# Optimization experiments

Measured on AMD Instinct MI355X. Metric: run time of the kernel, lower is better.

Reference implementation:

```python
import jax, jax.numpy as jnp
import numpy as np

H = 256; NL = 6; N = 64; DCONV = 4; DIN = 512; HEADS = 8; P = 64
CONVD = DIN + 2 * N            # 640
PROJ = 2 * DIN + 2 * N + HEADS  # 1160


def rmsnorm(x, w, eps=1e-6):
    return x * jax.lax.rsqrt(jnp.mean(x * x, axis=-1, keepdims=True) + eps) * w


def mamba2(x, Win, conv_w, conv_b, dt_bias, A_log, D, gnorm, Wout):
    # x: (b, l, H)
    b, l, _ = x.shape
    zxbcdt = x @ Win                       # (b, l, PROJ)
    z = zxbcdt[..., :DIN]
    xBC = zxbcdt[..., DIN:DIN + CONVD]
    dt = zxbcdt[..., DIN + CONVD:]         # (b, l, HEADS)
    # causal depthwise conv1d along l
    xp = jnp.pad(xBC, ((0, 0), (DCONV - 1, 0), (0, 0)))
    xc = conv_b + sum(xp[:, k:k + l, :] * conv_w[k] for k in range(DCONV))
    xBC = jax.nn.silu(xc)
    xs = xBC[..., :DIN]
    B = xBC[..., DIN:DIN + N]
    C = xBC[..., DIN + N:]
    dt = jax.nn.softplus(dt + dt_bias)
    dA = jnp.exp(dt * (-jnp.exp(A_log)))   # (b, l, HEADS)
    xh = xs.reshape(b, l, HEADS, P)
    xdt = xh * dt[..., None]

    def step(h, inp):
        dA_t, xdt_t, B_t, C_t = inp
        h = dA_t[:, :, None, None] * h + xdt_t[..., None] * B_t[:, None, None, :]
        return h, jnp.einsum('bhpn,bn->bhp', h, C_t)

    h0 = jnp.zeros((b, HEADS, P, N), x.dtype)
    _, ys = jax.lax.scan(step, h0, (jnp.swapaxes(dA, 0, 1), jnp.swapaxes(xdt, 0, 1),
                                    jnp.swapaxes(B, 0, 1), jnp.swapaxes(C, 0, 1)))
    y = jnp.swapaxes(ys, 0, 1) + D[None, None, :, None] * xh   # (b, l, HEADS, P)
    y = y.reshape(b, l, DIN) * jax.nn.silu(z)
    return rmsnorm(y, gnorm) @ Wout


def dual_path(x, t_norm, t_Win, t_cw, t_cb, t_dtb, t_Alog, t_D, t_gn, t_Wout,
              b_norm, b_Win, b_cw, b_cb, b_dtb, b_Alog, b_D, b_gn, b_Wout):
    batch, time, bands, hdim = x.shape
    for i in range(NL):
        # time-axis pass (raw row-major reshape, matching torch .reshape semantics)
        xt = x.reshape(batch * bands, time, hdim)
        xt = xt + mamba2(rmsnorm(xt, t_norm[i]), t_Win[i], t_cw[i], t_cb[i],
                         t_dtb[i], t_Alog[i], t_D[i], t_gn[i], t_Wout[i])
        x = jnp.swapaxes(xt.reshape(batch, bands, time, hdim), 1, 2)
        # band-axis pass
        xb = x.reshape(batch * time, bands, hdim)
        xb = xb + mamba2(rmsnorm(xb, b_norm[i]), b_Win[i], b_cw[i], b_cb[i],
                         b_dtb[i], b_Alog[i], b_D[i], b_gn[i], b_Wout[i])
        x = xb.reshape(batch, time, bands, hdim)
    return x


def setup_inputs() -> dict:
    key = jax.random.key(0)
    ks = jax.random.split(key, 3)
    x = jax.random.normal(ks[0], (2, 512, 64, H), jnp.float32)

    def make_params(k):
        kk = jax.random.split(k, 5)
        g = lambda kx, sh, s: jax.random.normal(kx, sh, jnp.float32) * s
        return dict(
            norm=jnp.ones((NL, H), jnp.float32),
            Win=g(kk[0], (NL, H, PROJ), H ** -0.5),
            cw=g(kk[1], (NL, DCONV, CONVD), 0.2),
            cb=jnp.zeros((NL, CONVD), jnp.float32),
            dtb=g(kk[2], (NL, HEADS), 0.5),
            Alog=jnp.log(jnp.abs(g(kk[3], (NL, HEADS), 1.0)) + 0.5),
            D=jnp.ones((NL, HEADS), jnp.float32),
            gn=jnp.ones((NL, DIN), jnp.float32),
            Wout=g(kk[4], (NL, DIN, H), DIN ** -0.5),
        )

    tp = make_params(ks[1]); bp = make_params(ks[2])
    out = {'x': x}
    for name, d in (('t', tp), ('b', bp)):
        for kname, v in d.items():
            out[f'{name}_{kname}'] = v
    return out


def reference(x, t_norm, t_Win, t_cw, t_cb, t_dtb, t_Alog, t_D, t_gn, t_Wout,
              b_norm, b_Win, b_cw, b_cb, b_dtb, b_Alog, b_D, b_gn, b_Wout):
    return dual_path(x, t_norm, t_Win, t_cw, t_cb, t_dtb, t_Alog, t_D, t_gn, t_Wout,
                     b_norm, b_Win, b_cw, b_cb, b_dtb, b_Alog, b_D, b_gn, b_Wout)
```

## Files before the change

kernel.cpp:

```cpp
#include <hip/hip_runtime.h>
#include <math.h>

#define NLAY   6
#define Hd     256
#define DINv   512
#define NHEADS 8
#define CONVDv 640
#define PROJv  1160
#define ZW     656
#define NTOK   65536
#define NCH    1024

typedef __attribute__((ext_vector_type(8))) short bf16x8;
typedef __attribute__((ext_vector_type(4))) float f32x4;
typedef unsigned short u16;

__device__ __forceinline__ float siluf(float v) {
    return v * __builtin_amdgcn_rcpf(1.0f + __expf(-v));
}
__device__ __forceinline__ float bflo(unsigned u) { return __uint_as_float(u << 16); }
__device__ __forceinline__ float bfhi(unsigned u) { return __uint_as_float(u & 0xffff0000u); }
__device__ __forceinline__ u16 f2b(float f) {
    unsigned u = __float_as_uint(f);
    return (u16)((u + 0x7fffu + ((u >> 16) & 1u)) >> 16);
}
__device__ __forceinline__ float b2f(u16 s) { return __uint_as_float(((unsigned)s) << 16); }

__device__ __forceinline__ void gl_lds16(const void* g, void* l) {
    __builtin_amdgcn_global_load_lds((const __attribute__((address_space(1))) unsigned int*)g,
                                     (__attribute__((address_space(3))) unsigned int*)l, 16, 0, 0);
}

__global__ __launch_bounds__(512)
void kprep_win(const float* __restrict__ tW, const float* __restrict__ bW,
               u16* __restrict__ Whi, u16* __restrict__ Wlo)
{
    const int li = blockIdx.y, j = blockIdx.x;
    const int t  = threadIdx.x;
    const int kk = t >> 6, col = (t >> 2) & 15, quad = t & 3;
    const float* W = (li < 6) ? (tW + (size_t)li * Hd * PROJv)
                              : (bW + (size_t)(li - 6) * Hd * PROJv);
    const int fullcol = 16 * j + col;
    const size_t ob = ((size_t)li * 74 + j) * 4096 + kk * 512 + quad * 128 + col * 8;
#pragma unroll
    for (int e = 0; e < 8; e++) {
        const int k = kk * 32 + quad * 8 + e;
        const float v = (fullcol < PROJv) ? W[(size_t)k * PROJv + fullcol] : 0.f;
        const u16 hi = f2b(v);
        Whi[ob + e] = hi;
        Wlo[ob + e] = f2b(v - b2f(hi));
    }
}

__global__ __launch_bounds__(512)
void kprep_wout(const float* __restrict__ tW, const float* __restrict__ tg,
                const float* __restrict__ bW, const float* __restrict__ bg,
                u16* __restrict__ Whi, u16* __restrict__ Wlo)
{
    const int li = blockIdx.y, j = blockIdx.x;
    const int t  = threadIdx.x;
    const int kk = t >> 5, col = (t >> 1) & 15, qh = t & 1;
    const float* W = (li < 6) ? tW + (size_t)li * DINv * Hd : bW + (size_t)(li - 6) * DINv * Hd;
    const float* g = (li < 6) ? tg + li * DINv : bg + (li - 6) * DINv;
    const int fullcol = 16 * j + col;
#pragma unroll
    for (int q = 0; q < 2; q++) {
        const int quad = qh * 2 + q;
        const size_t ob = ((size_t)li * 16 + j) * 8192 + kk * 512 + quad * 128 + col * 8;
#pragma unroll
        for (int e = 0; e < 8; e++) {
            const int k = kk * 32 + quad * 8 + e;
            const float v = W[(size_t)k * Hd + fullcol] * g[k];
            const u16 hi = f2b(v);
            Whi[ob + e] = hi;
            Wlo[ob + e] = f2b(v - b2f(hi));
        }
    }
}

__global__ __launch_bounds__(512, 4)
void k1_mfma(const float* __restrict__ src, u16* __restrict__ zs,
             u16* __restrict__ xrawT, u16* __restrict__ bnd,
             const float* __restrict__ nw,
             const u16* __restrict__ Whi, const u16* __restrict__ Wlo)
{
    __shared__ __align__(16) char smem[67584];
    u16* sAh = (u16*)smem;
    u16* sAl = sAh + 64 * 264;
    const int tid = threadIdx.x;
    const int cb  = blockIdx.x;
    const int R0  = cb * 64;

    {
        const int tok = tid >> 3, l8 = tid & 7;
        const float* xr = src + ((size_t)(R0 + tok)) * Hd + l8 * 32;
        float vv[32];
#pragma unroll
        for (int q = 0; q < 8; q++) {
            float4 v = ((const float4*)xr)[q];
            vv[4*q] = v.x; vv[4*q+1] = v.y; vv[4*q+2] = v.z; vv[4*q+3] = v.w;
        }
        float ss = 0.f;
#pragma unroll
        for (int j = 0; j < 32; j++) ss += vv[j] * vv[j];
#pragma unroll
        for (int m = 4; m >= 1; m >>= 1) ss += __shfl_xor(ss, m, 8);
        const float rstd = rsqrtf(ss * (1.0f / Hd) + 1e-6f);
        const float* nr = nw + l8 * 32;
        u16* dh = sAh + tok * 264 + l8 * 32;
        u16* dl = sAl + tok * 264 + l8 * 32;
#pragma unroll
        for (int j = 0; j < 32; j++) {
            const float val = vv[j] * rstd * nr[j];
            const u16 hi = f2b(val);
            dh[j] = hi;
            dl[j] = f2b(val - b2f(hi));
        }
    }
    __syncthreads();

    const int lane = tid & 63, wave = tid >> 6;
    const int rh = wave >> 1, cw = wave & 1;
    const int quad = lane >> 4, m16 = lane & 15;

    bf16x8 ah[8], al[8];
    {
        const u16* ph = sAh + (rh * 16 + m16) * 264 + quad * 8;
        const u16* pl = sAl + (rh * 16 + m16) * 264 + quad * 8;
#pragma unroll
        for (int kk = 0; kk < 8; kk++) {
            ah[kk] = *(const bf16x8*)(ph + kk * 32);
            al[kk] = *(const bf16x8*)(pl + kk * 32);
        }
    }
    __syncthreads();

    u16* sW = (u16*)smem;

#define K1_STAGE(p, buf)                                                          \
    {                                                                             \
        const int obase = wave * 4096;                                            \
        _Pragma("unroll")                                                         \
        for (int i = 0; i < 4; i++) {                                             \
            const int o = obase + i * 1024;                                       \
            const int chunk = o >> 13, t2 = chunk >> 1, hl = chunk & 1;           \
            const int within = o & 8191;                                          \
            const u16* sbase = (hl ? Wlo : Whi) + (size_t)(2 * (p) + t2) * 4096;  \
            gl_lds16((const char*)sbase + within + lane * 16,                     \
                     (char*)sW + (buf) * 32768 + o);                              \
        }                                                                         \
    }

    K1_STAGE(0, 0);
    __syncthreads();

    for (int p = 0; p < 37; p++) {
        if (p < 36) K1_STAGE(p + 1, (p + 1) & 1);
        const int j = 2 * p + cw;
        const u16* tb = sW + (p & 1) * 16384 + cw * 8192 + lane * 8;
        f32x4 acc = (f32x4){0.f, 0.f, 0.f, 0.f};
#pragma unroll
        for (int kk = 0; kk < 8; kk++) {
            bf16x8 bh = *(const bf16x8*)(tb + kk * 512);
            bf16x8 bl = *(const bf16x8*)(tb + 4096 + kk * 512);
            acc = __builtin_amdgcn_mfma_f32_16x16x32_bf16(ah[kk], bh, acc, 0, 0, 0);
            acc = __builtin_amdgcn_mfma_f32_16x16x32_bf16(al[kk], bh, acc, 0, 0, 0);
            acc = __builtin_amdgcn_mfma_f32_16x16x32_bf16(ah[kk], bl, acc, 0, 0, 0);
        }
        const int fullcol = 16 * j + m16;
        if (j < 32) {
            u16* zr = zs + (size_t)(R0 + rh * 16 + quad * 4) * ZW + fullcol;
#pragma unroll
            for (int i = 0; i < 4; i++) zr[(size_t)i * ZW] = f2b(acc[i]);
        } else if (j < 64) {
            const int ch = fullcol - 512;
            uint2 v;
            v.x = (unsigned)f2b(acc[0]) | ((unsigned)f2b(acc[1]) << 16);
            v.y = (unsigned)f2b(acc[2]) | ((unsigned)f2b(acc[3]) << 16);
            *(uint2*)(xrawT + ((size_t)cb * 512 + ch) * 64 + rh * 16 + quad * 4) = v;
            if (rh == 3 && quad == 3) {
#pragma unroll
                for (int i = 1; i < 4; i++)
                    bnd[((size_t)cb * 3 + (i - 1)) * 640 + ch] = f2b(acc[i]);
            }
        } else if (j < 73) {
            const int zc = fullcol - 512;
            u16* zr = zs + (size_t)(R0 + rh * 16 + quad * 4) * ZW + zc;
#pragma unroll
            for (int i = 0; i < 4; i++) zr[(size_t)i * ZW] = f2b(acc[i]);
            if (j < 72 && rh == 3 && quad == 3) {
#pragma unroll
                for (int i = 1; i < 4; i++)
                    bnd[((size_t)cb * 3 + (i - 1)) * 640 + zc] = f2b(acc[i]);
            }
        }
        __syncthreads();
    }
#undef K1_STAGE
}

__device__ __forceinline__ void conv32_rmw(u16* xp, float w0, float w1, float w2, float w3,
                                           float bias, float h3, float h2, float h1)
{
    uint4 va = ((const uint4*)xp)[0], vb = ((const uint4*)xp)[1],
          vc = ((const uint4*)xp)[2], vd = ((const uint4*)xp)[3];
    unsigned uu[16] = {va.x, va.y, va.z, va.w, vb.x, vb.y, vb.z, vb.w,
                       vc.x, vc.y, vc.z, vc.w, vd.x, vd.y, vd.z, vd.w};
    unsigned ou[16];
#pragma unroll
    for (int k = 0; k < 16; k++) {
        const float x0 = bflo(uu[k]);
        const u16 o0 = f2b(siluf(bias + w0*h3 + w1*h2 + w2*h1 + w3*x0));
        h3 = h2; h2 = h1; h1 = x0;
        const float x1 = bfhi(uu[k]);
        const u16 o1 = f2b(siluf(bias + w0*h3 + w1*h2 + w2*h1 + w3*x1));
        h3 = h2; h2 = h1; h1 = x1;
        ou[k] = (unsigned)o0 | ((unsigned)o1 << 16);
    }
    ((uint4*)xp)[0] = make_uint4(ou[0],  ou[1],  ou[2],  ou[3]);
    ((uint4*)xp)[1] = make_uint4(ou[4],  ou[5],  ou[6],  ou[7]);
    ((uint4*)xp)[2] = make_uint4(ou[8],  ou[9],  ou[10], ou[11]);
    ((uint4*)xp)[3] = make_uint4(ou[12], ou[13], ou[14], ou[15]);
}

__global__ __launch_bounds__(256, 4)
void k2a_conv(u16* __restrict__ zs, u16* __restrict__ xrawT,
              float* __restrict__ spb, const u16* __restrict__ bnd,
              const float* __restrict__ cwp, const float* __restrict__ cbp,
              const float* __restrict__ dtbp, const float* __restrict__ alogp, int L)
{
    __shared__ __align__(16) u16 sBC[64][128];
    const int tid = threadIdx.x;
    const int cb  = blockIdx.x;
    const size_t row0 = (size_t)cb * 64;
    const bool atStart = (((int)(row0 % (size_t)L)) == 0);
    const int lane = tid & 63, wave = tid >> 6;

#pragma unroll
    for (int j = 0; j < 4; j++) {
        const int t0 = wave * 16 + j * 4;
        gl_lds16(zs + (row0 + t0 + (lane >> 4)) * ZW + 512 + (lane & 15) * 8,
                 (char*)sBC + t0 * 256);
    }

#pragma unroll
    for (int cc = 0; cc < 2; cc++) {
        const int ch = tid + cc * 256;
        const float w0 = cwp[0*CONVDv + ch], w1 = cwp[1*CONVDv + ch],
                    w2 = cwp[2*CONVDv + ch], w3 = cwp[3*CONVDv + ch];
        u16* xp = xrawT + ((size_t)cb * 512 + ch) * 64 + 32;
        const uint2 hv = *(const uint2*)(xp - 4);
        conv32_rmw(xp, w0, w1, w2, w3, cbp[ch], bfhi(hv.x), bflo(hv.y), bfhi(hv.y));
    }

    if (tid < 64) {
        const int t = tid;
        const uint4 dv = *(const uint4*)(zs + (row0 + t) * ZW + 640);
        const unsigned uu[4] = {dv.x, dv.y, dv.z, dv.w};
        float sp[8], ld[8];
#pragma unroll
        for (int h = 0; h < 8; h++) {
            const float d = ((h & 1) ? bfhi(uu[h >> 1]) : bflo(uu[h >> 1])) + dtbp[h];
            const float s = (d > 20.f) ? d : __logf(1.f + __expf(d));
            sp[h] = s;
            ld[h] = -__expf(alogp[h]) * s;
        }
        float* ob = spb + (row0 + t) * 24;
        *(float4*)(ob)      = make_float4(sp[0], sp[1], sp[2], sp[3]);
        *(float4*)(ob + 4)  = make_float4(sp[4], sp[5], sp[6], sp[7]);
        *(float4*)(ob + 8)  = make_float4(ld[0], ld[1], ld[2], ld[3]);
        *(float4*)(ob + 12) = make_float4(ld[4], ld[5], ld[6], ld[7]);
    }
    __syncthreads();

#pragma unroll
    for (int cc = 0; cc < 2; cc++) {
        const int ch = tid + cc * 256;
        const float w0 = cwp[0*CONVDv + ch], w1 = cwp[1*CONVDv + ch],
                    w2 = cwp[2*CONVDv + ch], w3 = cwp[3*CONVDv + ch];
        float h1 = 0.f, h2 = 0.f, h3 = 0.f;
        if (!atStart) {
            const u16* bp = bnd + ((size_t)(cb - 1) * 3) * 640 + ch;
            h3 = b2f(bp[0]); h2 = b2f(bp[640]); h1 = b2f(bp[1280]);
        }
        conv32_rmw(xrawT + ((size_t)cb * 512 + ch) * 64, w0, w1, w2, w3, cbp[ch], h3, h2, h1);
    }

    u16 o[32];
    {
        const int ch  = tid & 127;
        const int th  = tid >> 7;
        const int t0  = th * 32;
        const int gch = 512 + ch;
        const float w0 = cwp[0*CONVDv + gch], w1 = cwp[1*CONVDv + gch],
                    w2 = cwp[2*CONVDv + gch], w3 = cwp[3*CONVDv + gch];
        const float bias = cbp[gch];
        float h1, h2, h3;
        if (th) {
            h3 = b2f(sBC[29][ch]); h2 = b2f(sBC[30][ch]); h1 = b2f(sBC[31][ch]);
        } else if (!atStart) {
            const u16* bp = bnd + ((size_t)(cb - 1) * 3) * 640 + gch;
            h3 = b2f(bp[0]); h2 = b2f(bp[640]); h1 = b2f(bp[1280]);
        } else { h1 = h2 = h3 = 0.f; }
#pragma unroll
        for (int t = 0; t < 32; t++) {
            const float xv = b2f(sBC[t0 + t][ch]);
            o[t] = f2b(siluf(bias + w0*h3 + w1*h2 + w2*h1 + w3*xv));
            h3 = h2; h2 = h1; h1 = xv;
        }
    }
    __syncthreads();
    {
        const int ch = tid & 127, t0 = (tid >> 7) * 32;
#pragma unroll
        for (int t = 0; t < 32; t++) sBC[t0 + t][ch] = o[t];
    }
    __syncthreads();
#pragma unroll
    for (int i = 0; i < 4; i++) {
        const int g = tid + i * 256;
        const int t = g >> 4, s16 = g & 15;
        *(uint4*)(zs + (row0 + t) * ZW + 512 + s16 * 8) = *(const uint4*)(&sBC[t][s16 * 8]);
    }
}

template<bool TMODE>
__global__ __launch_bounds__(256, 3)
void k2b_ssd(u16* __restrict__ zs, u16* __restrict__ xrawT,
             float* __restrict__ spb, u16* __restrict__ Sbuf,
             const float* __restrict__ Dp)
{
    __shared__ __align__(16) float sG[64][68];
    __shared__ float sClog[NHEADS][64];
    __shared__ float sSp[NHEADS][64];
    __shared__ float sWd[NHEADS][64];
    __shared__ __align__(16) u16 sBT[64][72];
    const int tid = threadIdx.x;
    const int lane = tid & 63, wave = tid >> 6;
    const int quad = lane >> 4, m16 = lane & 15;
    const int cb = blockIdx.x;
    const size_t row0 = (size_t)cb * 64;

    if (TMODE) {
        const int t_ = tid >> 2, ns = (tid & 3) * 16;
        const u16* br = zs + (row0 + t_) * ZW + 512 + ns;
        uint4 a = ((const uint4*)br)[0], b = ((const uint4*)br)[1];
        unsigned uu[8] = {a.x, a.y, a.z, a.w, b.x, b.y, b.z, b.w};
#pragma unroll
        for (int k = 0; k < 8; k++) {
            sBT[ns + 2*k][t_]     = (u16)(uu[k] & 0xffff);
            sBT[ns + 2*k + 1][t_] = (u16)(uu[k] >> 16);
        }
    }

    {
        const u16* cp = zs + (row0 + 16 * wave + m16) * ZW + 576 + quad * 8;
        bf16x8 cf0 = *(const bf16x8*)(cp);
        bf16x8 cf1 = *(const bf16x8*)(cp + 32);
#pragma unroll
        for (int st = 0; st < 4; st++) {
            const u16* bp = zs + (row0 + 16 * st + m16) * ZW + 512 + quad * 8;
            f32x4 acc = (f32x4){0.f, 0.f, 0.f, 0.f};
            acc = __builtin_amdgcn_mfma_f32_16x16x32_bf16(cf0, *(const bf16x8*)(bp), acc, 0, 0, 0);
            acc = __builtin_amdgcn_mfma_f32_16x16x32_bf16(cf1, *(const bf16x8*)(bp + 32), acc, 0, 0, 0);
#pragma unroll
            for (int i = 0; i < 4; i++)
                sG[16 * wave + quad * 4 + i][16 * st + m16] = acc[i];
        }
    }

#pragma unroll
    for (int hh = 0; hh < 2; hh++) {
        const int h = wave * 2 + hh;
        float c = spb[(row0 + lane) * 24 + 8 + h];
        const float sp = spb[(row0 + lane) * 24 + h];
#pragma unroll
        for (int d = 1; d < 64; d <<= 1) {
            const float o = __shfl_up(c, d, 64);
            if (lane >= d) c += o;
        }
        sClog[h][lane] = c;
        sSp[h][lane] = sp;
        if (TMODE) {
            spb[(row0 + lane) * 24 + 16 + h] = __expf(c);
            const float cl63 = __shfl(c, 63, 64);
            sWd[h][lane] = __expf(cl63 - c) * sp;
        }
    }
    __syncthreads();

    if (TMODE) {
        for (int h = 0; h < NHEADS; h++) {
            bf16x8 Ahi[2], Alo[2];
#pragma unroll
            for (int kk = 0; kk < 2; kk++) {
                const u16* xp = xrawT + ((size_t)cb * 512 + h * 64 + 16 * wave + m16) * 64
                                + 32 * kk + quad * 8;
                bf16x8 xf = *(const bf16x8*)xp;
                const float* wp = &sWd[h][32 * kk + quad * 8];
#pragma unroll
                for (int j = 0; j < 8; j++) {
                    const float v = b2f((u16)xf[j]) * wp[j];
                    const u16 hi = f2b(v);
                    Ahi[kk][j] = (short)hi;
                    Alo[kk][j] = (short)f2b(v - b2f(hi));
                }
            }
            u16* sb = Sbuf + ((size_t)cb * 8 + h) * 4096;
#pragma unroll
            for (int nt = 0; nt < 4; nt++) {
                f32x4 acc = (f32x4){0.f, 0.f, 0.f, 0.f};
#pragma unroll
                for (int kk = 0; kk < 2; kk++) {
                    const bf16x8 bf_ = *(const bf16x8*)(&sBT[16 * nt + m16][32 * kk + quad * 8]);
                    acc = __builtin_amdgcn_mfma_f32_16x16x32_bf16(Ahi[kk], bf_, acc, 0, 0, 0);
                    acc = __builtin_amdgcn_mfma_f32_16x16x32_bf16(Alo[kk], bf_, acc, 0, 0, 0);
                }
#pragma unroll
                for (int i = 0; i < 4; i++)
                    sb[(16 * wave + quad * 4 + i) * 64 + 16 * nt + m16] = f2b(acc[i]);
            }
        }
        __syncthreads();
    }

    const int t = 16 * wave + m16;
    for (int h = 0; h < NHEADS; h++) {
        const float Dh = Dp[h];
        const float clt = sClog[h][t];
        bf16x8 Mhi[2], Mlo[2];
#pragma unroll
        for (int kk = 0; kk < 2; kk++) {
            const float* gp = &sG[t][32 * kk + quad * 8];
            const float* cp = &sClog[h][32 * kk + quad * 8];
            const float* pp = &sSp[h][32 * kk + quad * 8];
#pragma unroll
            for (int j = 0; j < 8; j++) {
                const int s = 32 * kk + quad * 8 + j;
                float m = (s <= t) ? (__expf(clt - cp[j]) * pp[j] * gp[j]) : 0.f;
                if (s == t) m += Dh;
                const u16 hi = f2b(m);
                Mhi[kk][j] = (short)hi;
                Mlo[kk][j] = (short)f2b(m - b2f(hi));
            }
        }
        bf16x8 xf[4][2];
#pragma unroll
        for (int pt = 0; pt < 4; pt++)
#pragma unroll
            for (int kk = 0; kk < 2; kk++)
                xf[pt][kk] = *(const bf16x8*)(xrawT
                    + ((size_t)cb * 512 + h * 64 + 16 * pt + m16) * 64 + 32 * kk + quad * 8);
        if (TMODE) __syncthreads();
        f32x4 accY[4];
#pragma unroll
        for (int pt = 0; pt < 4; pt++) {
            accY[pt] = (f32x4){0.f, 0.f, 0.f, 0.f};
#pragma unroll
            for (int kk = 0; kk < 2; kk++) {
                accY[pt] = __builtin_amdgcn_mfma_f32_16x16x32_bf16(Mhi[kk], xf[pt][kk], accY[pt], 0, 0, 0);
                accY[pt] = __builtin_amdgcn_mfma_f32_16x16x32_bf16(Mlo[kk], xf[pt][kk], accY[pt], 0, 0, 0);
            }
        }
#pragma unroll
        for (int pt = 0; pt < 4; pt++) {
            if (TMODE) {
                uint2 v;
                v.x = (unsigned)f2b(accY[pt][0]) | ((unsigned)f2b(accY[pt][1]) << 16);
                v.y = (unsigned)f2b(accY[pt][2]) | ((unsigned)f2b(accY[pt][3]) << 16);
                *(uint2*)(xrawT + ((size_t)cb * 512 + h * 64 + 16 * pt + m16) * 64
                          + 16 * wave + quad * 4) = v;
            } else {
#pragma unroll
                for (int i = 0; i < 4; i++) {
                    const size_t row = row0 + 16 * wave + quad * 4 + i;
                    const int col = h * 64 + 16 * pt + m16;
                    const u16 zv = zs[row * ZW + col];
                    zs[row * ZW + col] = f2b(accY[pt][i] * siluf(b2f(zv)));
                }
            }
        }
    }
}

__global__ __launch_bounds__(64, 4)
void k2c_states(u16* __restrict__ Sbuf, const float* __restrict__ spb)
{
    const int p = threadIdx.x, h = blockIdx.y, s = blockIdx.x;
    float H[64];
#pragma unroll
    for (int n = 0; n < 64; n++) H[n] = 0.f;
    for (int c = 1; c < 8; c++) {
        const float P = spb[((size_t)s * 512 + (c - 1) * 64 + 63) * 24 + 16 + h];
        u16* sp_ = Sbuf + (((size_t)(s * 8 + c - 1) * 8 + h) * 4096) + p * 64;
#pragma unroll
        for (int n = 0; n < 64; n += 8) {
            uint4 v = *(const uint4*)(sp_ + n);
            unsigned uu[4] = {v.x, v.y, v.z, v.w};
            float sv[8];
#pragma unroll
            for (int w2 = 0; w2 < 4; w2++) { sv[2*w2] = bflo(uu[w2]); sv[2*w2+1] = bfhi(uu[w2]); }
#pragma unroll
            for (int e = 0; e < 8; e++) H[n + e] = fmaf(P, H[n + e], sv[e]);
            uint4 o;
            o.x = (unsigned)f2b(H[n+0]) | ((unsigned)f2b(H[n+1]) << 16);
            o.y = (unsigned)f2b(H[n+2]) | ((unsigned)f2b(H[n+3]) << 16);
            o.z = (unsigned)f2b(H[n+4]) | ((unsigned)f2b(H[n+5]) << 16);
            o.w = (unsigned)f2b(H[n+6]) | ((unsigned)f2b(H[n+7]) << 16);
            *(uint4*)(sp_ + n) = o;
        }
    }
}

__global__ __launch_bounds__(256, 4)
void k2d_corr(u16* __restrict__ zs, const u16* __restrict__ xrawT,
              const float* __restrict__ spb, const u16* __restrict__ Sbuf)
{
    const int tid = threadIdx.x;
    const int lane = tid & 63, wave = tid >> 6;
    const int quad = lane >> 4, m16 = lane & 15;
    const int cb = blockIdx.x;
    const int c = cb & 7;
    const size_t row0 = (size_t)cb * 64;

    for (int h = 0; h < NHEADS; h++) {
        f32x4 acc[4];
#pragma unroll
        for (int pt = 0; pt < 4; pt++) {
            const uint2 v = *(const uint2*)(xrawT
                + ((size_t)cb * 512 + h * 64 + 16 * pt + m16) * 64 + 16 * wave + quad * 4);
            acc[pt][0] = bflo(v.x); acc[pt][1] = bfhi(v.x);
            acc[pt][2] = bflo(v.y); acc[pt][3] = bfhi(v.y);
        }
        if (c) {
            const float at = spb[(row0 + 16 * wave + m16) * 24 + 16 + h];
            bf16x8 Ahi[2], Alo[2];
#pragma unroll
            for (int kk = 0; kk < 2; kk++) {
                const u16* cp = zs + (row0 + 16 * wave + m16) * ZW + 576 + 32 * kk + quad * 8;
                bf16x8 cf = *(const bf16x8*)cp;
#pragma unroll
                for (int j = 0; j < 8; j++) {
                    const float v = b2f((u16)cf[j]) * at;
                    const u16 hi = f2b(v);
                    Ahi[kk][j] = (short)hi;
                    Alo[kk][j] = (short)f2b(v - b2f(hi));
                }
            }
            const u16* hb = Sbuf + ((size_t)(cb - 1) * 8 + h) * 4096;
#pragma unroll
            for (int pt = 0; pt < 4; pt++) {
#pragma unroll
                for (int kk = 0; kk < 2; kk++) {
                    bf16x8 hf = *(const bf16x8*)(hb + (16 * pt + m16) * 64 + 32 * kk + quad * 8);
                    acc[pt] = __builtin_amdgcn_mfma_f32_16x16x32_bf16(Ahi[kk], hf, acc[pt], 0, 0, 0);
                    acc[pt] = __builtin_amdgcn_mfma_f32_16x16x32_bf16(Alo[kk], hf, acc[pt], 0, 0, 0);
                }
            }
        }
#pragma unroll
        for (int pt = 0; pt < 4; pt++) {
#pragma unroll
            for (int i = 0; i < 4; i++) {
                const size_t row = row0 + 16 * wave + quad * 4 + i;
                const int col = h * 64 + 16 * pt + m16;
                const u16 zv = zs[row * ZW + col];
                zs[row * ZW + col] = f2b(acc[pt][i] * siluf(b2f(zv)));
            }
        }
    }
}

template<bool TMODE>
__global__ __launch_bounds__(256, 2)
void k3_mfma(const u16* __restrict__ zs, const float* __restrict__ src,
             float* __restrict__ dst,
             const u16* __restrict__ Whi, const u16* __restrict__ Wlo)
{
    __shared__ __align__(16) char smem[32768];
    const int tid = threadIdx.x;
    const int cb  = blockIdx.x;
    const int R0  = cb * 64;
    const int lane = tid & 63, wave = tid >> 6;
    const int quad = lane >> 4, m16 = lane & 15;

#define K3_STAGE(hc)                                                              \
    {                                                                             \
        const int jj = (hc) >> 1;                                                 \
        const char* wb = (const char*)((((hc) & 1) ? Wlo : Whi) + (size_t)jj * 8192); \
        char* db = smem + ((hc) & 1) * 16384 + wave * 4096;                       \
        _Pragma("unroll")                                                         \
        for (int i = 0; i < 4; i++)                                               \
            gl_lds16(wb + wave * 4096 + i * 1024 + lane * 16, db + i * 1024);     \
    }

    K3_STAGE(0);

    const u16* yr = zs + (size_t)(R0 + wave * 16 + m16) * ZW + quad * 8;
    float ss = 0.f;
#pragma unroll
    for (int kk = 0; kk < 16; kk++) {
        uint4 u = *(const uint4*)(yr + kk * 32);
        float a;
        a = bflo(u.x); ss += a * a;  a = bfhi(u.x); ss += a * a;
        a = bflo(u.y); ss += a * a;  a = bfhi(u.y); ss += a * a;
        a = bflo(u.z); ss += a * a;  a = bfhi(u.z); ss += a * a;
        a = bflo(u.w); ss += a * a;  a = bfhi(u.w); ss += a * a;
    }
    ss += __shfl_xor(ss, 16, 64);
    ss += __shfl_xor(ss, 32, 64);
    const float rstd = rsqrtf(ss * (1.0f / DINv) + 1e-6f);

    bf16x8 ah[16], al[16];
#pragma unroll
    for (int kk = 0; kk < 16; kk++) {
        uint4 u = *(const uint4*)(yr + kk * 32);
        unsigned w0 = u.x, w1 = u.y, w2 = u.z, w3 = u.w;
        float a, b;
        u16 hi;
        a = bflo(w0) * rstd; b = bfhi(w0) * rstd;
        hi = f2b(a); ah[kk][0] = (short)hi; al[kk][0] = (short)f2b(a - b2f(hi));
        hi = f2b(b); ah[kk][1] = (short)hi; al[kk][1] = (short)f2b(b - b2f(hi));
        a = bflo(w1) * rstd; b = bfhi(w1) * rstd;
        hi = f2b(a); ah[kk][2] = (short)hi; al[kk][2] = (short)f2b(a - b2f(hi));
        hi = f2b(b); ah[kk][3] = (short)hi; al[kk][3] = (short)f2b(b - b2f(hi));
        a = bflo(w2) * rstd; b = bfhi(w2) * rstd;
        hi = f2b(a); ah[kk][4] = (short)hi; al[kk][4] = (short)f2b(a - b2f(hi));
        hi = f2b(b); ah[kk][5] = (short)hi; al[kk][5] = (short)f2b(b - b2f(hi));
        a = bflo(w3) * rstd; b = bfhi(w3) * rstd;
        hi = f2b(a); ah[kk][6] = (short)hi; al[kk][6] = (short)f2b(a - b2f(hi));
        hi = f2b(b); ah[kk][7] = (short)hi; al[kk][7] = (short)f2b(b - b2f(hi));
    }
    __syncthreads();

    for (int j = 0; j < 16; j++) {
        K3_STAGE(2 * j + 1);
        f32x4 acc = (f32x4){0.f, 0.f, 0.f, 0.f};
        const u16* tb0 = (const u16*)smem + lane * 8;
#pragma unroll
        for (int kk = 0; kk < 16; kk++) {
            bf16x8 bh = *(const bf16x8*)(tb0 + kk * 512);
            acc = __builtin_amdgcn_mfma_f32_16x16x32_bf16(ah[kk], bh, acc, 0, 0, 0);
            acc = __builtin_amdgcn_mfma_f32_16x16x32_bf16(al[kk], bh, acc, 0, 0, 0);
        }
        __syncthreads();
        if (j < 15) K3_STAGE(2 * j + 2);
        const u16* tb1 = (const u16*)(smem + 16384) + lane * 8;
#pragma unroll
        for (int kk = 0; kk < 16; kk++) {
            bf16x8 bl = *(const bf16x8*)(tb1 + kk * 512);
            acc = __builtin_amdgcn_mfma_f32_16x16x32_bf16(ah[kk], bl, acc, 0, 0, 0);
        }
        {
            const int col = 16 * j + m16;
#pragma unroll
            for (int i = 0; i < 4; i++) {
                const size_t inrow = (size_t)(R0 + wave * 16 + quad * 4 + i);
                const float v = acc[i] + src[inrow * Hd + col];
                size_t orow;
                if (TMODE) {
                    const size_t sq = inrow >> 9;
                    const size_t tt = inrow & 511;
                    orow = ((sq >> 6) * 512 + tt) * 64 + (sq & 63);
                } else {
                    orow = inrow;
                }
                dst[orow * Hd + col] = v;
            }
        }
        __syncthreads();
    }
#undef K3_STAGE
}

extern "C" void kernel_launch(void* const* d_in, const int* in_sizes, int n_in,
                              void* d_out, int out_size, void* d_ws, size_t ws_size,
                              hipStream_t stream) {
    const float* x      = (const float*)d_in[0];
    const float* t_norm = (const float*)d_in[1];
    const float* t_Win  = (const float*)d_in[2];
    const float* t_cw   = (const float*)d_in[3];
    const float* t_cb   = (const float*)d_in[4];
    const float* t_dtb  = (const float*)d_in[5];
    const float* t_Alog = (const float*)d_in[6];
    const float* t_D    = (const float*)d_in[7];
    const float* t_gn   = (const float*)d_in[8];
    const float* t_Wout = (const float*)d_in[9];
    const float* b_norm = (const float*)d_in[10];
    const float* b_Win  = (const float*)d_in[11];
    const float* b_cw   = (const float*)d_in[12];
    const float* b_cb   = (const float*)d_in[13];
    const float* b_dtb  = (const float*)d_in[14];
    const float* b_Alog = (const float*)d_in[15];
    const float* b_D    = (const float*)d_in[16];
    const float* b_gn   = (const float*)d_in[17];
    const float* b_Wout = (const float*)d_in[18];

    float* out = (float*)d_out;
    char*  wsb = (char*)d_ws;
    float* xbuf = (float*)wsb;
    u16*   Sbuf = (u16*)wsb;
    size_t off = 67108864;
    u16* W1hi = (u16*)(wsb + off); off += (size_t)12 * 74 * 4096 * 2;
    u16* W1lo = (u16*)(wsb + off); off += (size_t)12 * 74 * 4096 * 2;
    u16* W2hi = (u16*)(wsb + off); off += (size_t)12 * 16 * 8192 * 2;
    u16* W2lo = (u16*)(wsb + off); off += (size_t)12 * 16 * 8192 * 2;
    u16* zs   = (u16*)(wsb + off); off += (size_t)NTOK * ZW * 2;
    float* spb = (float*)(wsb + off); off += (size_t)NTOK * 24 * 4;
    u16* xrawT = (u16*)(wsb + off); off += (size_t)NTOK * 512 * 2;
    u16* bnd  = (u16*)(wsb + off);

    kprep_win<<<dim3(74, 12), 512, 0, stream>>>(t_Win, b_Win, W1hi, W1lo);
    kprep_wout<<<dim3(16, 12), 512, 0, stream>>>(t_Wout, t_gn, b_Wout, b_gn, W2hi, W2lo);

    for (int i = 0; i < NLAY; i++) {
        const float* src_t = (i == 0) ? x : out;
        k1_mfma<<<NCH, 512, 0, stream>>>(src_t, zs, xrawT, bnd, t_norm + i * Hd,
                 W1hi + (size_t)i * 74 * 4096, W1lo + (size_t)i * 74 * 4096);
        k2a_conv<<<NCH, 256, 0, stream>>>(zs, xrawT, spb, bnd,
                 t_cw + i * 4 * CONVDv, t_cb + i * CONVDv, t_dtb + i * NHEADS,
                 t_Alog + i * NHEADS, 512);
        k2b_ssd<true><<<NCH, 256, 0, stream>>>(zs, xrawT, spb, Sbuf, t_D + i * NHEADS);
        k2c_states<<<dim3(128, NHEADS), 64, 0, stream>>>(Sbuf, spb);
        k2d_corr<<<NCH, 256, 0, stream>>>(zs, xrawT, spb, Sbuf);
        k3_mfma<true><<<NCH, 256, 0, stream>>>(zs, src_t, xbuf,
                 W2hi + (size_t)i * 16 * 8192, W2lo + (size_t)i * 16 * 8192);
        k1_mfma<<<NCH, 512, 0, stream>>>(xbuf, zs, xrawT, bnd, b_norm + i * Hd,
                 W1hi + (size_t)(i + 6) * 74 * 4096, W1lo + (size_t)(i + 6) * 74 * 4096);
        k2a_conv<<<NCH, 256, 0, stream>>>(zs, xrawT, spb, bnd,
                 b_cw + i * 4 * CONVDv, b_cb + i * CONVDv, b_dtb + i * NHEADS,
                 b_Alog + i * NHEADS, 64);
        k2b_ssd<false><<<NCH, 256, 0, stream>>>(zs, xrawT, spb, Sbuf, b_D + i * NHEADS);
        k3_mfma<false><<<NCH, 256, 0, stream>>>(zs, xbuf, out,
                 W2hi + (size_t)(i + 6) * 16 * 8192, W2lo + (size_t)(i + 6) * 16 * 8192);
    }
}
```

Measured before the change: 5.304 ms.

## Halve k1 block to 4 waves, each computing two row tiles per weight fragment

The input-projection kernel now runs 256 threads per block. Each wave covers 32 rows (two 16-row MFMA tiles), so every weight fragment read from LDS feeds twice as many MFMAs. The RMSNorm and bf16 hi/lo split are computed straight into registers from global memory, removing the LDS staging buffer and a barrier. In exchange, each thread loads twice as much weight data per stage, register pressure doubles for the A fragments, and fewer waves are resident to hide latency.

New measurement: 5.838 ms. +10.1%, slower.

```diff
diff --git a/kernel.cpp b/kernel.cpp
--- a/kernel.cpp
+++ b/kernel.cpp
@@ -78,70 +78,27 @@
     }
 }
 
-__global__ __launch_bounds__(512, 4)
+__global__ __launch_bounds__(256, 2)
 void k1_mfma(const float* __restrict__ src, u16* __restrict__ zs,
              u16* __restrict__ xrawT, u16* __restrict__ bnd,
              const float* __restrict__ nw,
              const u16* __restrict__ Whi, const u16* __restrict__ Wlo)
 {
-    __shared__ __align__(16) char smem[67584];
-    u16* sAh = (u16*)smem;
-    u16* sAl = sAh + 64 * 264;
+    __shared__ __align__(16) char smem[65536];
     const int tid = threadIdx.x;
     const int cb  = blockIdx.x;
     const int R0  = cb * 64;
-
-    {
-        const int tok = tid >> 3, l8 = tid & 7;
-        const float* xr = src + ((size_t)(R0 + tok)) * Hd + l8 * 32;
-        float vv[32];
-#pragma unroll
-        for (int q = 0; q < 8; q++) {
-            float4 v = ((const float4*)xr)[q];
-            vv[4*q] = v.x; vv[4*q+1] = v.y; vv[4*q+2] = v.z; vv[4*q+3] = v.w;
-        }
-        float ss = 0.f;
-#pragma unroll
-        for (int j = 0; j < 32; j++) ss += vv[j] * vv[j];
-#pragma unroll
-        for (int m = 4; m >= 1; m >>= 1) ss += __shfl_xor(ss, m, 8);
-        const float rstd = rsqrtf(ss * (1.0f / Hd) + 1e-6f);
-        const float* nr = nw + l8 * 32;
-        u16* dh = sAh + tok * 264 + l8 * 32;
-        u16* dl = sAl + tok * 264 + l8 * 32;
-#pragma unroll
-        for (int j = 0; j < 32; j++) {
-            const float val = vv[j] * rstd * nr[j];
-            const u16 hi = f2b(val);
-            dh[j] = hi;
-            dl[j] = f2b(val - b2f(hi));
-        }
-    }
-    __syncthreads();
-
     const int lane = tid & 63, wave = tid >> 6;
-    const int rh = wave >> 1, cw = wave & 1;
     const int quad = lane >> 4, m16 = lane & 15;
-
-    bf16x8 ah[8], al[8];
-    {
-        const u16* ph = sAh + (rh * 16 + m16) * 264 + quad * 8;
-        const u16* pl = sAl + (rh * 16 + m16) * 264 + quad * 8;
-#pragma unroll
-        for (int kk = 0; kk < 8; kk++) {
-            ah[kk] = *(const bf16x8*)(ph + kk * 32);
-            al[kk] = *(const bf16x8*)(pl + kk * 32);
-        }
-    }
-    __syncthreads();
+    const int rg = wave >> 1, cw = wave & 1;
 
     u16* sW = (u16*)smem;
 
 #define K1_STAGE(p, buf)                                                          \
     {                                                                             \
-        const int obase = wave * 4096;                                            \
+        const int obase = wave * 8192;                                            \
         _Pragma("unroll")                                                         \
-        for (int i = 0; i < 4; i++) {                                             \
+        for (int i = 0; i < 8; i++) {                                             \
             const int o = obase + i * 1024;                                       \
             const int chunk = o >> 13, t2 = chunk >> 1, hl = chunk & 1;           \
             const int within = o & 8191;                                          \
@@ -152,46 +109,88 @@
     }
 
     K1_STAGE(0, 0);
+
+    bf16x8 ah[2][8], al[2][8];
+#pragma unroll
+    for (int s = 0; s < 2; s++) {
+        const float* xr = src + (size_t)(R0 + rg * 32 + s * 16 + m16) * Hd + quad * 8;
+        float ss = 0.f;
+#pragma unroll
+        for (int kk = 0; kk < 8; kk++) {
+            float4 fa = ((const float4*)(xr + kk * 32))[0];
+            float4 fb = ((const float4*)(xr + kk * 32))[1];
+            ss += fa.x*fa.x + fa.y*fa.y + fa.z*fa.z + fa.w*fa.w;
+            ss += fb.x*fb.x + fb.y*fb.y + fb.z*fb.z + fb.w*fb.w;
+        }
+        ss += __shfl_xor(ss, 16, 64);
+        ss += __shfl_xor(ss, 32, 64);
+        const float rstd = rsqrtf(ss * (1.0f / Hd) + 1e-6f);
+#pragma unroll
+        for (int kk = 0; kk < 8; kk++) {
+            float4 fa = ((const float4*)(xr + kk * 32))[0];
+            float4 fb = ((const float4*)(xr + kk * 32))[1];
+            float4 na = ((const float4*)(nw + kk * 32 + quad * 8))[0];
+            float4 nb = ((const float4*)(nw + kk * 32 + quad * 8))[1];
+            const float f[8] = {fa.x*na.x, fa.y*na.y, fa.z*na.z, fa.w*na.w,
+                                fb.x*nb.x, fb.y*nb.y, fb.z*nb.z, fb.w*nb.w};
+#pragma unroll
+            for (int e = 0; e < 8; e++) {
+                const float v = f[e] * rstd;
+                const u16 hi = f2b(v);
+                ah[s][kk][e] = (short)hi;
+                al[s][kk][e] = (short)f2b(v - b2f(hi));
+            }
+        }
+    }
     __syncthreads();
 
     for (int p = 0; p < 37; p++) {
         if (p < 36) K1_STAGE(p + 1, (p + 1) & 1);
         const int j = 2 * p + cw;
         const u16* tb = sW + (p & 1) * 16384 + cw * 8192 + lane * 8;
-        f32x4 acc = (f32x4){0.f, 0.f, 0.f, 0.f};
+        f32x4 acc[2];
+        acc[0] = (f32x4){0.f, 0.f, 0.f, 0.f};
+        acc[1] = (f32x4){0.f, 0.f, 0.f, 0.f};
 #pragma unroll
         for (int kk = 0; kk < 8; kk++) {
             bf16x8 bh = *(const bf16x8*)(tb + kk * 512);
             bf16x8 bl = *(const bf16x8*)(tb + 4096 + kk * 512);
-            acc = __builtin_amdgcn_mfma_f32_16x16x32_bf16(ah[kk], bh, acc, 0, 0, 0);
-            acc = __builtin_amdgcn_mfma_f32_16x16x32_bf16(al[kk], bh, acc, 0, 0, 0);
-            acc = __builtin_amdgcn_mfma_f32_16x16x32_bf16(ah[kk], bl, acc, 0, 0, 0);
+            acc[0] = __builtin_amdgcn_mfma_f32_16x16x32_bf16(ah[0][kk], bh, acc[0], 0, 0, 0);
+            acc[0] = __builtin_amdgcn_mfma_f32_16x16x32_bf16(al[0][kk], bh, acc[0], 0, 0, 0);
+            acc[0] = __builtin_amdgcn_mfma_f32_16x16x32_bf16(ah[0][kk], bl, acc[0], 0, 0, 0);
+            acc[1] = __builtin_amdgcn_mfma_f32_16x16x32_bf16(ah[1][kk], bh, acc[1], 0, 0, 0);
+            acc[1] = __builtin_amdgcn_mfma_f32_16x16x32_bf16(al[1][kk], bh, acc[1], 0, 0, 0);
+            acc[1] = __builtin_amdgcn_mfma_f32_16x16x32_bf16(ah[1][kk], bl, acc[1], 0, 0, 0);
         }
         const int fullcol = 16 * j + m16;
-        if (j < 32) {
-            u16* zr = zs + (size_t)(R0 + rh * 16 + quad * 4) * ZW + fullcol;
-#pragma unroll
-            for (int i = 0; i < 4; i++) zr[(size_t)i * ZW] = f2b(acc[i]);
-        } else if (j < 64) {
-            const int ch = fullcol - 512;
-            uint2 v;
-            v.x = (unsigned)f2b(acc[0]) | ((unsigned)f2b(acc[1]) << 16);
-            v.y = (unsigned)f2b(acc[2]) | ((unsigned)f2b(acc[3]) << 16);
-            *(uint2*)(xrawT + ((size_t)cb * 512 + ch) * 64 + rh * 16 + quad * 4) = v;
-            if (rh == 3 && quad == 3) {
-#pragma unroll
-                for (int i = 1; i < 4; i++)
-                    bnd[((size_t)cb * 3 + (i - 1)) * 640 + ch] = f2b(acc[i]);
-            }
-        } else if (j < 73) {
-            const int zc = fullcol - 512;
-            u16* zr = zs + (size_t)(R0 + rh * 16 + quad * 4) * ZW + zc;
-#pragma unroll
-            for (int i = 0; i < 4; i++) zr[(size_t)i * ZW] = f2b(acc[i]);
-            if (j < 72 && rh == 3 && quad == 3) {
-#pragma unroll
-                for (int i = 1; i < 4; i++)
-                    bnd[((size_t)cb * 3 + (i - 1)) * 640 + zc] = f2b(acc[i]);
+#pragma unroll
+        for (int s = 0; s < 2; s++) {
+            const int rbase = rg * 32 + s * 16 + quad * 4;
+            if (j < 32) {
+                u16* zr = zs + (size_t)(R0 + rbase) * ZW + fullcol;
+#pragma unroll
+                for (int i = 0; i < 4; i++) zr[(size_t)i * ZW] = f2b(acc[s][i]);
+            } else if (j < 64) {
+                const int ch = fullcol - 512;
+                uint2 v;
+                v.x = (unsigned)f2b(acc[s][0]) | ((unsigned)f2b(acc[s][1]) << 16);
+                v.y = (unsigned)f2b(acc[s][2]) | ((unsigned)f2b(acc[s][3]) << 16);
+                *(uint2*)(xrawT + ((size_t)cb * 512 + ch) * 64 + rbase) = v;
+                if (rg == 1 && s == 1 && quad == 3) {
+#pragma unroll
+                    for (int i = 1; i < 4; i++)
+                        bnd[((size_t)cb * 3 + (i - 1)) * 640 + ch] = f2b(acc[s][i]);
+                }
+            } else if (j < 73) {
+                const int zc = fullcol - 512;
+                u16* zr = zs + (size_t)(R0 + rbase) * ZW + zc;
+#pragma unroll
+                for (int i = 0; i < 4; i++) zr[(size_t)i * ZW] = f2b(acc[s][i]);
+                if (j < 72 && rg == 1 && s == 1 && quad == 3) {
+#pragma unroll
+                    for (int i = 1; i < 4; i++)
+                        bnd[((size_t)cb * 3 + (i - 1)) * 640 + zc] = f2b(acc[s][i]);
+                }
             }
         }
         __syncthreads();
@@ -715,7 +714,7 @@
 
     for (int i = 0; i < NLAY; i++) {
         const float* src_t = (i == 0) ? x : out;
-        k1_mfma<<<NCH, 512, 0, stream>>>(src_t, zs, xrawT, bnd, t_norm + i * Hd,
+        k1_mfma<<<NCH, 256, 0, stream>>>(src_t, zs, xrawT, bnd, t_norm + i * Hd,
                  W1hi + (size_t)i * 74 * 4096, W1lo + (size_t)i * 74 * 4096);
         k2a_conv<<<NCH, 256, 0, stream>>>(zs, xrawT, spb, bnd,
                  t_cw + i * 4 * CONVDv, t_cb + i * CONVDv, t_dtb + i * NHEADS,
@@ -725,7 +724,7 @@
         k2d_corr<<<NCH, 256, 0, stream>>>(zs, xrawT, spb, Sbuf);
         k3_mfma<true><<<NCH, 256, 0, stream>>>(zs, src_t, xbuf,
                  W2hi + (size_t)i * 16 * 8192, W2lo + (size_t)i * 16 * 8192);
-        k1_mfma<<<NCH, 512, 0, stream>>>(xbuf, zs, xrawT, bnd, b_norm + i * Hd,
+        k1_mfma<<<NCH, 256, 0, stream>>>(xbuf, zs, xrawT, bnd, b_norm + i * Hd,
                  W1hi + (size_t)(i + 6) * 74 * 4096, W1lo + (size_t)(i + 6) * 74 * 4096);
         k2a_conv<<<NCH, 256, 0, stream>>>(zs, xrawT, spb, bnd,
                  b_cw + i * 4 * CONVDv, b_cb + i * CONVDv, b_dtb + i * NHEADS,
```
